# Kernel tuning notes

Hardware: AMD Instinct MI355X
Metric: run time of the kernel (lower is better)

## Reference

```python
import jax, jax.numpy as jnp
import numpy as np

B, S, H = 2, 2048, 1024
E, K, I, IS = 8, 2, 1408, 2816

def setup_inputs() -> dict:
    key = jax.random.key(0)
    ks = jax.random.split(key, 9)
    sc = lambda fan_in: 1.0 / np.sqrt(fan_in)
    return {
        'hidden_states': jax.random.normal(ks[0], (B, S, H), jnp.float32),
        'gate_w': jax.random.normal(ks[1], (H, E), jnp.float32) * sc(H),
        'w_gate': jax.random.normal(ks[2], (E, H, I), jnp.float32) * sc(H),
        'w_up': jax.random.normal(ks[3], (E, H, I), jnp.float32) * sc(H),
        'w_down': jax.random.normal(ks[4], (E, I, H), jnp.float32) * sc(I),
        'sh_gate_w': jax.random.normal(ks[5], (H, IS), jnp.float32) * sc(H),
        'sh_up_w': jax.random.normal(ks[6], (H, IS), jnp.float32) * sc(H),
        'sh_down_w': jax.random.normal(ks[7], (IS, H), jnp.float32) * sc(IS),
        'sh_expert_gate_w': jax.random.normal(ks[8], (H, 1), jnp.float32) * sc(H),
        'top_k': K,
    }

def reference(hidden_states, gate_w, w_gate, w_up, w_down, sh_gate_w, sh_up_w, sh_down_w, sh_expert_gate_w, top_k):
    orig_shape = hidden_states.shape
    x = hidden_states.reshape(-1, orig_shape[-1])  # [T, H]
    T = x.shape[0]
    n_experts = gate_w.shape[1]
    # --- routing (matches _route_single_token, no expert_bias) ---
    logits = x @ gate_w                               # [T, E]
    topk_vals, topk_ids = jax.lax.top_k(logits, top_k)  # [T, K]
    topk_weights = jax.nn.softmax(topk_vals, axis=-1)   # [T, K]
    # dense routing matrix [T, E]; each token has K nonzeros
    route = jnp.zeros((T, n_experts), x.dtype).at[jnp.arange(T)[:, None], topk_ids].add(topk_weights)
    # --- expert SwiGLU FFNs, masked-combine over the fixed expert set ---
    out = jnp.zeros_like(x)
    for e in range(n_experts):
        h = jax.nn.silu(x @ w_gate[e]) * (x @ w_up[e])  # [T, I]
        out = out + route[:, e:e + 1] * (h @ w_down[e])
    # --- shared expert (always active) with sigmoid gate ---
    shared = (jax.nn.silu(x @ sh_gate_w) * (x @ sh_up_w)) @ sh_down_w
    shared = jax.nn.sigmoid(x @ sh_expert_gate_w) * shared
    out = out + shared
    return out.reshape(orig_shape)
```

## Files before the change

### kernel.cpp

```cpp
#include <hip/hip_runtime.h>
#include <hip/hip_bf16.h>

#define T_TOK 4096
#define HDIM  1024
#define NEXP  8
#define IDIM  1408
#define ISDIM 2816
#define PADT  10240

typedef short bf16x8 __attribute__((ext_vector_type(8)));
typedef float f32x4  __attribute__((ext_vector_type(4)));
typedef unsigned short u16;
typedef unsigned short u16x4 __attribute__((ext_vector_type(4)));
typedef unsigned short u16x8 __attribute__((ext_vector_type(8)));

typedef __attribute__((address_space(1))) const void gvoid;
typedef __attribute__((address_space(3))) void lvoid;

__device__ __forceinline__ u16 f2bf(float f) {
    union { float f; unsigned u; } c; c.f = f;
    unsigned r = (c.u + 0x7FFFu + ((c.u >> 16) & 1u)) >> 16;
    return (u16)r;
}
__device__ __forceinline__ float bf2f(u16 v) {
    union { unsigned u; float f; } c; c.u = (unsigned)v << 16; return c.f;
}
__device__ __forceinline__ void glds16(const u16* g, u16* l) {
    __builtin_amdgcn_global_load_lds((gvoid*)g, (lvoid*)l, 16, 0, 0);
}

__global__ __launch_bounds__(256) void route_kernel(
    const float* __restrict__ X, const float* __restrict__ GW,
    const float* __restrict__ SEG,
    int* __restrict__ topk_e, float* __restrict__ topk_w,
    float* __restrict__ sgate)
{
    const int t = blockIdx.x * 4 + (threadIdx.x >> 6);
    const int lane = threadIdx.x & 63;
    float acc[NEXP];
    #pragma unroll
    for (int e = 0; e < NEXP; ++e) acc[e] = 0.f;
    float sacc = 0.f;
    const float* xr = X + (size_t)t * HDIM;
    for (int h = lane; h < HDIM; h += 64) {
        float xv = xr[h];
        f32x4 g0 = *(const f32x4*)(GW + (size_t)h * NEXP);
        f32x4 g1 = *(const f32x4*)(GW + (size_t)h * NEXP + 4);
        acc[0] += xv * g0[0]; acc[1] += xv * g0[1];
        acc[2] += xv * g0[2]; acc[3] += xv * g0[3];
        acc[4] += xv * g1[0]; acc[5] += xv * g1[1];
        acc[6] += xv * g1[2]; acc[7] += xv * g1[3];
        sacc += xv * SEG[h];
    }
    #pragma unroll
    for (int off = 32; off > 0; off >>= 1) {
        #pragma unroll
        for (int e = 0; e < NEXP; ++e) acc[e] += __shfl_down(acc[e], off);
        sacc += __shfl_down(sacc, off);
    }
    if (lane == 0) {
        int e0 = 0;
        #pragma unroll
        for (int e = 1; e < NEXP; ++e) if (acc[e] > acc[e0]) e0 = e;
        int e1 = (e0 == 0) ? 1 : 0;
        #pragma unroll
        for (int e = 0; e < NEXP; ++e)
            if (e != e0 && acc[e] > acc[e1]) e1 = e;
        float w0 = 1.f / (1.f + __expf(acc[e1] - acc[e0]));
        topk_e[t * 2]     = e0; topk_e[t * 2 + 1] = e1;
        topk_w[t * 2]     = w0; topk_w[t * 2 + 1] = 1.f - w0;
        sgate[t] = 1.f / (1.f + __expf(-sacc));
    }
}

__global__ __launch_bounds__(256) void hist_kernel(
    const int* __restrict__ topk_e, int* __restrict__ counts)
{
    __shared__ int h[NEXP];
    if (threadIdx.x < NEXP) h[threadIdx.x] = 0;
    __syncthreads();
    int i = blockIdx.x * 256 + threadIdx.x;
    atomicAdd(&h[topk_e[i]], 1);
    __syncthreads();
    if (threadIdx.x < NEXP) atomicAdd(&counts[threadIdx.x], h[threadIdx.x]);
}

__global__ void offsets_kernel(const int* __restrict__ counts,
                               int* __restrict__ seg_pad,
                               int* __restrict__ cursors)
{
    if (threadIdx.x == 0) {
        int s = 0;
        for (int e = 0; e < NEXP; ++e) {
            seg_pad[e] = s; cursors[e] = s;
            s += ((counts[e] + 255) >> 8) << 8;
        }
        seg_pad[NEXP] = s;
    }
}

__global__ __launch_bounds__(256) void prefill_kernel(int* __restrict__ tok_ids)
{
    int i = blockIdx.x * 256 + threadIdx.x;
    if (i < PADT) tok_ids[i] = 0;
}

__global__ __launch_bounds__(256) void scatter_kernel(
    const int* __restrict__ topk_e,
    int* __restrict__ cursors, int* __restrict__ tok_ids,
    int* __restrict__ slot)
{
    const int i = blockIdx.x * 256 + threadIdx.x;
    const int lane = threadIdx.x & 63;
    const int e = topk_e[i];
    const unsigned long long lt = (1ull << lane) - 1ull;
    #pragma unroll
    for (int ex = 0; ex < NEXP; ++ex) {
        unsigned long long mask = __ballot(e == ex);
        if (mask == 0ull) continue;
        int cnt = __popcll(mask);
        int leader = __ffsll((long long)mask) - 1;
        int base_ = 0;
        if (lane == leader) base_ = atomicAdd(&cursors[ex], cnt);
        base_ = __shfl(base_, leader);
        if (e == ex) {
            int pos = base_ + __popcll(mask & lt);
            tok_ids[pos] = i >> 1;
            slot[i] = pos;
        }
    }
}

__global__ __launch_bounds__(256) void cvt_x_kernel(
    const float* __restrict__ in, u16* __restrict__ out, int n)
{
    int i = (blockIdx.x * 256 + threadIdx.x) * 8;
    if (i < n) {
        f32x4 a = *(const f32x4*)(in + i);
        f32x4 b = *(const f32x4*)(in + i + 4);
        u16x8 o;
        #pragma unroll
        for (int j = 0; j < 4; ++j) { o[j] = f2bf(a[j]); o[j + 4] = f2bf(b[j]); }
        *(u16x8*)(out + i) = o;
    }
}

__global__ __launch_bounds__(256) void transpose_cvt(
    const float* __restrict__ in0, const float* __restrict__ in1,
    u16* __restrict__ out, int K, int N, int split, int ilv)
{
    const int z = blockIdx.z;
    const int e = (z < split) ? z : z - split;
    const float* in = (z < split) ? (in0 + (size_t)z * K * N)
                                  : (in1 + (size_t)(z - split) * K * N);
    u16* o = ilv ? (out + (size_t)e * 2 * N * K)
                 : (out + (size_t)z * N * K);
    const int radd = ilv ? ((z < split) ? 0 : 16) : 0;

    __shared__ float tile[64][65];
    const int n0 = blockIdx.x * 64, k0 = blockIdx.y * 64;
    const int tx = threadIdx.x & 15;
    const int ty = threadIdx.x >> 4;

    #pragma unroll
    for (int p = 0; p < 4; ++p) {
        int k = ty + p * 16;
        f32x4 v = *(const f32x4*)(in + (size_t)(k0 + k) * N + n0 + tx * 4);
        *(f32x4*)&tile[k][tx * 4] = v;
    }
    __syncthreads();
    #pragma unroll
    for (int p = 0; p < 4; ++p) {
        int n = ty + p * 16;
        u16x4 w;
        #pragma unroll
        for (int j = 0; j < 4; ++j) w[j] = f2bf(tile[tx * 4 + j][n]);
        int R = n0 + n;
        int orow = ilv ? (((R >> 4) * 32) + (R & 15) + radd) : R;
        *(u16x4*)(o + (size_t)orow * K + k0 + tx * 4) = w;
    }
}


#define BAR() __builtin_amdgcn_s_barrier()
#define WCNT0() asm volatile("s_waitcnt vmcnt(0)" ::: "memory")

#define GSTAGE(wb) do { \
    glds16(aP, &As[(wb) + tid * 8]); \
    glds16(bP, &Bs[(wb) + tid * 8]); \
    aP += 32; bP += 32; } while (0)

#define GEMM_TILE(rb) { \
    bf16x8 av[4], bv[4]; \
    _Pragma("unroll") for (int q = 0; q < 4; ++q) bv[q] = *(const bf16x8*)&Bs[(rb) + bofs[q]]; \
    _Pragma("unroll") for (int q = 0; q < 4; ++q) av[q] = *(const bf16x8*)&As[(rb) + aofs[q]]; \
    __builtin_amdgcn_s_setprio(1); \
    _Pragma("unroll") for (int q = 0; q < 4; ++q) \
        _Pragma("unroll") for (int w = 0; w < 4; ++w) \
            acc[q][w] = __builtin_amdgcn_mfma_f32_16x16x32_bf16(av[q], bv[w], acc[q][w], 0, 0, 0); \
    __builtin_amdgcn_s_setprio(0); }

#define GEMM_MAIN(NT) \
    GSTAGE(0); \
    _Pragma("unroll 1") \
    for (int t = 0; t < (NT) - 1; ++t) { \
        WCNT0(); BAR(); \
        GSTAGE((t & 1) ? 0 : 8192); \
        GEMM_TILE((t & 1) * 8192) \
    } \
    WCNT0(); BAR(); \
    GEMM_TILE((((NT) - 1) & 1) * 8192)

__global__ __launch_bounds__(1024, 4) void gemm_gu(
    const u16* __restrict__ A,
    const u16* __restrict__ WGUc, const u16* __restrict__ SGUc,
    u16* __restrict__ HoutE, u16* __restrict__ HoutS,
    const int* __restrict__ tok_ids, const int* __restrict__ seg_pad)
{
    extern __shared__ u16 lds[];
    u16* As = lds;
    u16* Bs = lds + 16384;

    const int zz = blockIdx.x;
    int m0, nblk, N;
    const u16* Bsrc;
    u16* Hout;
    bool gather;
    if (zz < 440) {
        int widx = zz / 11;
        nblk = zz - widx * 11;
        m0 = widx * 256;
        if (m0 >= seg_pad[NEXP]) return;
        int e = 0;
        while (e < 7 && m0 >= seg_pad[e + 1]) ++e;
        Bsrc = WGUc + (size_t)e * (2 * IDIM * HDIM);
        Hout = HoutE; N = IDIM; gather = true;
    } else {
        int sidx = zz - 440;
        int mz = sidx / 22;
        nblk = sidx - mz * 22;
        m0 = mz * 256;
        Bsrc = SGUc; Hout = HoutS; N = ISDIM; gather = false;
    }

    const int tid = threadIdx.x;
    const int srow = tid >> 2;
    const int sk = (((tid & 3) ^ ((tid >> 3) & 3))) * 8;
    const int arow = m0 + srow;
    const int ga = gather ? tok_ids[arow] : arow;
    const u16* aP = A + (size_t)ga * HDIM + sk;
    const u16* bP = Bsrc + (size_t)(nblk * 256 + srow) * HDIM + sk;

    f32x4 acc[4][4];
    #pragma unroll
    for (int i = 0; i < 4; ++i)
        #pragma unroll
        for (int j = 0; j < 4; ++j) acc[i][j] = (f32x4){0.f, 0.f, 0.f, 0.f};

    const int lane = tid & 63;
    const int wv = tid >> 6;
    const int wr = wv >> 2;
    const int wn = wv & 3;
    const int l15 = lane & 15;
    const int ksl = lane >> 4;
    const int kswz = ((ksl ^ ((l15 >> 1) & 3))) * 8;
    int aofs[4], bofs[4];
    #pragma unroll
    for (int q = 0; q < 4; ++q) {
        aofs[q] = (wr * 64 + q * 16 + l15) * 32 + kswz;
        bofs[q] = (wn * 64 + q * 16 + l15) * 32 + kswz;
    }

    GEMM_MAIN(32)

    const int l4 = ksl * 4;
    #pragma unroll
    for (int j = 0; j < 4; ++j)
        #pragma unroll
        for (int p = 0; p < 2; ++p) {
            f32x4 g = acc[j][2 * p], u = acc[j][2 * p + 1];
            int c = nblk * 128 + (wn * 2 + p) * 16 + l15;
            #pragma unroll
            for (int jj = 0; jj < 4; ++jj) {
                int r = m0 + wr * 64 + j * 16 + l4 + jj;
                float hv = g[jj] / (1.f + __expf(-g[jj])) * u[jj];
                Hout[(size_t)r * N + c] = f2bf(hv);
            }
        }
}

__global__ __launch_bounds__(1024, 4) void gemm_down(
    const u16* __restrict__ AE, const u16* __restrict__ AS,
    const u16* __restrict__ WDt, const u16* __restrict__ SDt,
    float* __restrict__ DexpO, float* __restrict__ OutS,
    const int* __restrict__ seg_pad)
{
    extern __shared__ u16 lds[];
    u16* As = lds;
    u16* Bs = lds + 16384;

    const int zz = blockIdx.x;
    const bool shr = (zz >= 160);
    int m0, n0, kst;
    size_t koff;
    const u16 *Asrc, *Bsrc;
    if (!shr) {
        int widx = zz >> 2;
        n0 = (zz & 3) * 256;
        m0 = widx * 256;
        if (m0 >= seg_pad[NEXP]) return;
        int e = 0;
        while (e < 7 && m0 >= seg_pad[e + 1]) ++e;
        Asrc = AE; Bsrc = WDt + (size_t)e * (HDIM * IDIM);
        kst = IDIM; koff = 0;
    } else {
        int idx = zz - 160;
        int kc = idx >> 6;
        int rem = idx & 63;
        m0 = (rem >> 2) * 256;
        n0 = (rem & 3) * 256;
        Asrc = AS; Bsrc = SDt;
        kst = ISDIM; koff = (size_t)kc * 1408;
    }

    const int tid = threadIdx.x;
    const int srow = tid >> 2;
    const int sk = (((tid & 3) ^ ((tid >> 3) & 3))) * 8;
    const u16* aP = Asrc + (size_t)(m0 + srow) * kst + koff + sk;
    const u16* bP = Bsrc + (size_t)(n0 + srow) * kst + koff + sk;

    f32x4 acc[4][4];
    #pragma unroll
    for (int i = 0; i < 4; ++i)
        #pragma unroll
        for (int j = 0; j < 4; ++j) acc[i][j] = (f32x4){0.f, 0.f, 0.f, 0.f};

    const int lane = tid & 63;
    const int wv = tid >> 6;
    const int wr = wv >> 2;
    const int wn = wv & 3;
    const int l15 = lane & 15;
    const int ksl = lane >> 4;
    const int kswz = ((ksl ^ ((l15 >> 1) & 3))) * 8;
    int aofs[4], bofs[4];
    #pragma unroll
    for (int q = 0; q < 4; ++q) {
        aofs[q] = (wr * 64 + q * 16 + l15) * 32 + kswz;
        bofs[q] = (wn * 64 + q * 16 + l15) * 32 + kswz;
    }

    GEMM_MAIN(44)

    const int l4 = ksl * 4;
    #pragma unroll
    for (int j = 0; j < 4; ++j)
        #pragma unroll
        for (int i = 0; i < 4; ++i) {
            int c = n0 + wn * 64 + i * 16 + l15;
            #pragma unroll
            for (int jj = 0; jj < 4; ++jj) {
                int r = m0 + wr * 64 + j * 16 + l4 + jj;
                if (!shr)
                    DexpO[(size_t)r * HDIM + c] = acc[j][i][jj];
                else
                    atomicAdd(&OutS[(size_t)r * HDIM + c], acc[j][i][jj]);
            }
        }
}

__global__ __launch_bounds__(256) void combine_kernel(
    const float* __restrict__ Dexp,
    const int* __restrict__ slot, const float* __restrict__ topk_w,
    const float* __restrict__ sgate, float* __restrict__ Out)
{
    int idx = blockIdx.x * 256 + threadIdx.x;
    int t = idx >> 8;
    int c = (idx & 255) * 4;
    int s0 = slot[2 * t], s1 = slot[2 * t + 1];
    float w0 = topk_w[2 * t], w1 = topk_w[2 * t + 1], sg = sgate[t];
    f32x4 sh = *(const f32x4*)(Out + (size_t)t * HDIM + c);
    f32x4 d0 = *(const f32x4*)(Dexp + (size_t)s0 * HDIM + c);
    f32x4 d1 = *(const f32x4*)(Dexp + (size_t)s1 * HDIM + c);
    f32x4 o;
    #pragma unroll
    for (int j = 0; j < 4; ++j) o[j] = sg * sh[j] + w0 * d0[j] + w1 * d1[j];
    *(f32x4*)(Out + (size_t)t * HDIM + c) = o;
}

extern "C" void kernel_launch(void* const* d_in, const int* in_sizes, int n_in,
                              void* d_out, int out_size, void* d_ws, size_t ws_size,
                              hipStream_t stream)
{
    const float* X   = (const float*)d_in[0];
    const float* GW  = (const float*)d_in[1];
    const float* WG  = (const float*)d_in[2];
    const float* WU  = (const float*)d_in[3];
    const float* WD  = (const float*)d_in[4];
    const float* SG  = (const float*)d_in[5];
    const float* SU  = (const float*)d_in[6];
    const float* SD  = (const float*)d_in[7];
    const float* SEG = (const float*)d_in[8];
    float* Out = (float*)d_out;

    char* ws = (char*)d_ws;
    int*   counts    = (int*)(ws + 0);
    int*   seg_pad   = (int*)(ws + 64);
    int*   cursors   = (int*)(ws + 128);
    int*   topk_e    = (int*)(ws + 1024);
    float* topk_w    = (float*)(ws + 1024 + 32768);
    float* sgate     = (float*)(ws + 1024 + 65536);
    int*   slot      = (int*)(ws + 1024 + 65536 + 16384);
    int*   tok_ids   = (int*)(ws + 1024 + 65536 + 16384 + 32768);

    u16* Xbf  = (u16*)(ws + 0x0040000ull);
    u16* Hact = (u16*)(ws + 0x0840000ull);
    u16* Hs   = (u16*)(ws + 0x23C0000ull);
    u16* WGUc = (u16*)(ws + 0x39C0000ull);
    u16* WDt  = (u16*)(ws + 0x65C0000ull);
    u16* SGUc = (u16*)(ws + 0x7BC0000ull);
    u16* SDt  = (u16*)(ws + 0x86C0000ull);
    float* Dexp = (float*)(ws + 0x39C0000ull);

    hipMemsetAsync(counts, 0, 64, stream);
    hipMemsetAsync(Out, 0, (size_t)T_TOK * HDIM * sizeof(float), stream);

    route_kernel<<<T_TOK / 4, 256, 0, stream>>>(X, GW, SEG, topk_e, topk_w, sgate);
    hist_kernel<<<(T_TOK * 2) / 256, 256, 0, stream>>>(topk_e, counts);
    offsets_kernel<<<1, 64, 0, stream>>>(counts, seg_pad, cursors);
    prefill_kernel<<<PADT / 256, 256, 0, stream>>>(tok_ids);
    scatter_kernel<<<(T_TOK * 2) / 256, 256, 0, stream>>>(topk_e, cursors, tok_ids, slot);

    cvt_x_kernel<<<(T_TOK * HDIM) / (256 * 8), 256, 0, stream>>>(X, Xbf, T_TOK * HDIM);
    transpose_cvt<<<dim3(IDIM / 64, HDIM / 64, 2 * NEXP), 256, 0, stream>>>(WG, WU, WGUc, HDIM, IDIM, NEXP, 1);
    transpose_cvt<<<dim3(HDIM / 64, IDIM / 64, NEXP), 256, 0, stream>>>(WD, WD, WDt, IDIM, HDIM, NEXP, 0);
    transpose_cvt<<<dim3(ISDIM / 64, HDIM / 64, 2), 256, 0, stream>>>(SG, SU, SGUc, HDIM, ISDIM, 1, 1);
    transpose_cvt<<<dim3(HDIM / 64, ISDIM / 64, 1), 256, 0, stream>>>(SD, SD, SDt, ISDIM, HDIM, 1, 0);

    gemm_gu<<<792, 1024, 65536, stream>>>(
        Xbf, WGUc, SGUc, Hact, Hs, tok_ids, seg_pad);

    gemm_down<<<288, 1024, 65536, stream>>>(
        Hact, Hs, WDt, SDt, Dexp, Out, seg_pad);

    combine_kernel<<<(T_TOK * HDIM / 4) / 256, 256, 0, stream>>>(
        Dexp, slot, topk_w, sgate, Out);
}
```

Before: 309.2 us.

## Remap MoE GEMM grids per expert and widen transpose-convert stores

The grouped gate/up and down GEMMs now launch a 2D grid with blockIdx.x as the expert index and blockIdx.y enumerating that expert's M and N tiles. Each block reads its expert directly from seg_pad instead of scanning segments. Shared-expert tiles are interleaved across the x dimension, which changes dispatch order and may spread work and weight reuse differently across CUs. Separately, the transpose-convert kernel writes 8 bf16 values per store instead of 4 to widen global writes. The new grid also launches more blocks that return early, and tiles past a fixed per-expert bound are dropped, which could lose work if routing is very imbalanced.

Result: slower. 321.3 us (+3.9%).

```diff
diff --git a/kernel.cpp b/kernel.cpp
--- a/kernel.cpp
+++ b/kernel.cpp
@@ -169,15 +169,17 @@
         *(f32x4*)&tile[k][tx * 4] = v;
     }
     __syncthreads();
-    #pragma unroll
-    for (int p = 0; p < 4; ++p) {
-        int n = ty + p * 16;
-        u16x4 w;
-        #pragma unroll
-        for (int j = 0; j < 4; ++j) w[j] = f2bf(tile[tx * 4 + j][n]);
+    const int kb = (threadIdx.x & 7) * 8;
+    const int nr = threadIdx.x >> 3;
+    #pragma unroll
+    for (int p = 0; p < 2; ++p) {
+        int n = nr + p * 32;
+        u16x8 w;
+        #pragma unroll
+        for (int j = 0; j < 8; ++j) w[j] = f2bf(tile[kb + j][n]);
         int R = n0 + n;
         int orow = ilv ? (((R >> 4) * 32) + (R & 15) + radd) : R;
-        *(u16x4*)(o + (size_t)orow * K + k0 + tx * 4) = w;
+        *(u16x8*)(o + (size_t)orow * K + k0 + kb) = w;
     }
 }
 
@@ -221,25 +223,27 @@
     u16* As = lds;
     u16* Bs = lds + 16384;
 
-    const int zz = blockIdx.x;
+    const int x = blockIdx.x;
+    const int y = blockIdx.y;
     int m0, nblk, N;
     const u16* Bsrc;
     u16* Hout;
     bool gather;
-    if (zz < 440) {
-        int widx = zz / 11;
-        nblk = zz - widx * 11;
-        m0 = widx * 256;
-        if (m0 >= seg_pad[NEXP]) return;
-        int e = 0;
-        while (e < 7 && m0 >= seg_pad[e + 1]) ++e;
-        Bsrc = WGUc + (size_t)e * (2 * IDIM * HDIM);
+    if (y < 176) {
+        int mt = (seg_pad[x + 1] - seg_pad[x]) >> 8;
+        if (mt == 0) return;
+        int n = y / mt;
+        if (n >= 11) return;
+        int m = y - n * mt;
+        nblk = n;
+        m0 = seg_pad[x] + m * 256;
+        Bsrc = WGUc + (size_t)x * (2 * IDIM * HDIM);
         Hout = HoutE; N = IDIM; gather = true;
     } else {
-        int sidx = zz - 440;
-        int mz = sidx / 22;
-        nblk = sidx - mz * 22;
-        m0 = mz * 256;
+        int yl = y - 176;
+        nblk = yl >> 1;
+        int ml = yl & 1;
+        m0 = (2 * x + ml) * 256;
         Bsrc = SGUc; Hout = HoutS; N = ISDIM; gather = false;
     }
 
@@ -299,26 +303,31 @@
     u16* As = lds;
     u16* Bs = lds + 16384;
 
-    const int zz = blockIdx.x;
-    const bool shr = (zz >= 160);
+    const int x = blockIdx.x;
+    const int y = blockIdx.y;
+    bool shr;
     int m0, n0, kst;
     size_t koff;
     const u16 *Asrc, *Bsrc;
-    if (!shr) {
-        int widx = zz >> 2;
-        n0 = (zz & 3) * 256;
-        m0 = widx * 256;
-        if (m0 >= seg_pad[NEXP]) return;
-        int e = 0;
-        while (e < 7 && m0 >= seg_pad[e + 1]) ++e;
-        Asrc = AE; Bsrc = WDt + (size_t)e * (HDIM * IDIM);
+    if (y < 64) {
+        shr = false;
+        int mt = (seg_pad[x + 1] - seg_pad[x]) >> 8;
+        if (mt == 0) return;
+        int n = y / mt;
+        if (n >= 4) return;
+        int m = y - n * mt;
+        m0 = seg_pad[x] + m * 256;
+        n0 = n * 256;
+        Asrc = AE; Bsrc = WDt + (size_t)x * (HDIM * IDIM);
         kst = IDIM; koff = 0;
     } else {
-        int idx = zz - 160;
-        int kc = idx >> 6;
-        int rem = idx & 63;
-        m0 = (rem >> 2) * 256;
-        n0 = (rem & 3) * 256;
+        shr = true;
+        int yl = y - 64;
+        int kc = yl >> 3;
+        int rem = yl & 7;
+        n0 = (rem >> 1) * 256;
+        int ml = rem & 1;
+        m0 = (2 * x + ml) * 256;
         Asrc = AS; Bsrc = SDt;
         kst = ISDIM; koff = (size_t)kc * 1408;
     }
@@ -436,10 +445,10 @@
     transpose_cvt<<<dim3(ISDIM / 64, HDIM / 64, 2), 256, 0, stream>>>(SG, SU, SGUc, HDIM, ISDIM, 1, 1);
     transpose_cvt<<<dim3(HDIM / 64, ISDIM / 64, 1), 256, 0, stream>>>(SD, SD, SDt, ISDIM, HDIM, 1, 0);
 
-    gemm_gu<<<792, 1024, 65536, stream>>>(
+    gemm_gu<<<dim3(8, 220), 1024, 65536, stream>>>(
         Xbf, WGUc, SGUc, Hact, Hs, tok_ids, seg_pad);
 
-    gemm_down<<<288, 1024, 65536, stream>>>(
+    gemm_down<<<dim3(8, 80), 1024, 65536, stream>>>(
         Hact, Hs, WDt, SDt, Dexp, Out, seg_pad);
 
     combine_kernel<<<(T_TOK * HDIM / 4) / 256, 256, 0, stream>>>(
```

## Fuse MoE combine into down-projection epilogue via weighted atomic scatter

Applied to the files above, without the earlier changes.

Removes the combine kernel and the Dexp intermediate buffer. The down GEMM now scales each expert row by its routing weight and atomically adds it into the output at the owning token, while the shared expert rows are scaled by the sigmoid gate. The prefill kernel is folded into the histogram kernel, which also zeroes the new per-slot weight array. The transpose-convert kernel now writes 8-wide bf16 vectors instead of 4-wide. This saves one launch and a full fp32 intermediate round trip, at the cost of more atomics, which also makes the summation order nondeterministic.

Result: slower. 372.3 us (+20.4%).

```diff
diff --git a/kernel.cpp b/kernel.cpp
--- a/kernel.cpp
+++ b/kernel.cpp
@@ -74,13 +74,15 @@
 }
 
 __global__ __launch_bounds__(256) void hist_kernel(
-    const int* __restrict__ topk_e, int* __restrict__ counts)
+    const int* __restrict__ topk_e, int* __restrict__ counts,
+    int* __restrict__ tok_ids, float* __restrict__ sw)
 {
     __shared__ int h[NEXP];
     if (threadIdx.x < NEXP) h[threadIdx.x] = 0;
     __syncthreads();
     int i = blockIdx.x * 256 + threadIdx.x;
     atomicAdd(&h[topk_e[i]], 1);
+    for (int j = i; j < PADT; j += gridDim.x * 256) { tok_ids[j] = 0; sw[j] = 0.f; }
     __syncthreads();
     if (threadIdx.x < NEXP) atomicAdd(&counts[threadIdx.x], h[threadIdx.x]);
 }
@@ -99,16 +101,10 @@
     }
 }
 
-__global__ __launch_bounds__(256) void prefill_kernel(int* __restrict__ tok_ids)
-{
-    int i = blockIdx.x * 256 + threadIdx.x;
-    if (i < PADT) tok_ids[i] = 0;
-}
-
 __global__ __launch_bounds__(256) void scatter_kernel(
-    const int* __restrict__ topk_e,
+    const int* __restrict__ topk_e, const float* __restrict__ topk_w,
     int* __restrict__ cursors, int* __restrict__ tok_ids,
-    int* __restrict__ slot)
+    float* __restrict__ sw)
 {
     const int i = blockIdx.x * 256 + threadIdx.x;
     const int lane = threadIdx.x & 63;
@@ -126,7 +122,7 @@
         if (e == ex) {
             int pos = base_ + __popcll(mask & lt);
             tok_ids[pos] = i >> 1;
-            slot[i] = pos;
+            sw[pos] = topk_w[i];
         }
     }
 }
@@ -169,15 +165,17 @@
         *(f32x4*)&tile[k][tx * 4] = v;
     }
     __syncthreads();
-    #pragma unroll
-    for (int p = 0; p < 4; ++p) {
-        int n = ty + p * 16;
-        u16x4 w;
-        #pragma unroll
-        for (int j = 0; j < 4; ++j) w[j] = f2bf(tile[tx * 4 + j][n]);
+    const int kb = (threadIdx.x & 7) * 8;
+    const int nr = threadIdx.x >> 3;
+    #pragma unroll
+    for (int p = 0; p < 2; ++p) {
+        int n = nr + p * 32;
+        u16x8 w;
+        #pragma unroll
+        for (int j = 0; j < 8; ++j) w[j] = f2bf(tile[kb + j][n]);
         int R = n0 + n;
         int orow = ilv ? (((R >> 4) * 32) + (R & 15) + radd) : R;
-        *(u16x4*)(o + (size_t)orow * K + k0 + tx * 4) = w;
+        *(u16x8*)(o + (size_t)orow * K + k0 + kb) = w;
     }
 }
 
@@ -292,7 +290,9 @@
 __global__ __launch_bounds__(1024, 4) void gemm_down(
     const u16* __restrict__ AE, const u16* __restrict__ AS,
     const u16* __restrict__ WDt, const u16* __restrict__ SDt,
-    float* __restrict__ DexpO, float* __restrict__ OutS,
+    float* __restrict__ Out,
+    const int* __restrict__ tok_ids, const float* __restrict__ sw,
+    const float* __restrict__ sgate,
     const int* __restrict__ seg_pad)
 {
     extern __shared__ u16 lds[];
@@ -360,31 +360,15 @@
             #pragma unroll
             for (int jj = 0; jj < 4; ++jj) {
                 int r = m0 + wr * 64 + j * 16 + l4 + jj;
-                if (!shr)
-                    DexpO[(size_t)r * HDIM + c] = acc[j][i][jj];
-                else
-                    atomicAdd(&OutS[(size_t)r * HDIM + c], acc[j][i][jj]);
+                if (!shr) {
+                    float w = sw[r];
+                    int tok = tok_ids[r];
+                    atomicAdd(&Out[(size_t)tok * HDIM + c], w * acc[j][i][jj]);
+                } else {
+                    atomicAdd(&Out[(size_t)r * HDIM + c], sgate[r] * acc[j][i][jj]);
+                }
             }
         }
-}
-
-__global__ __launch_bounds__(256) void combine_kernel(
-    const float* __restrict__ Dexp,
-    const int* __restrict__ slot, const float* __restrict__ topk_w,
-    const float* __restrict__ sgate, float* __restrict__ Out)
-{
-    int idx = blockIdx.x * 256 + threadIdx.x;
-    int t = idx >> 8;
-    int c = (idx & 255) * 4;
-    int s0 = slot[2 * t], s1 = slot[2 * t + 1];
-    float w0 = topk_w[2 * t], w1 = topk_w[2 * t + 1], sg = sgate[t];
-    f32x4 sh = *(const f32x4*)(Out + (size_t)t * HDIM + c);
-    f32x4 d0 = *(const f32x4*)(Dexp + (size_t)s0 * HDIM + c);
-    f32x4 d1 = *(const f32x4*)(Dexp + (size_t)s1 * HDIM + c);
-    f32x4 o;
-    #pragma unroll
-    for (int j = 0; j < 4; ++j) o[j] = sg * sh[j] + w0 * d0[j] + w1 * d1[j];
-    *(f32x4*)(Out + (size_t)t * HDIM + c) = o;
 }
 
 extern "C" void kernel_launch(void* const* d_in, const int* in_sizes, int n_in,
@@ -409,8 +393,8 @@
     int*   topk_e    = (int*)(ws + 1024);
     float* topk_w    = (float*)(ws + 1024 + 32768);
     float* sgate     = (float*)(ws + 1024 + 65536);
-    int*   slot      = (int*)(ws + 1024 + 65536 + 16384);
-    int*   tok_ids   = (int*)(ws + 1024 + 65536 + 16384 + 32768);
+    int*   tok_ids   = (int*)(ws + 1024 + 65536 + 16384);
+    float* sw        = (float*)(ws + 1024 + 65536 + 16384 + 40960);
 
     u16* Xbf  = (u16*)(ws + 0x0040000ull);
     u16* Hact = (u16*)(ws + 0x0840000ull);
@@ -419,16 +403,14 @@
     u16* WDt  = (u16*)(ws + 0x65C0000ull);
     u16* SGUc = (u16*)(ws + 0x7BC0000ull);
     u16* SDt  = (u16*)(ws + 0x86C0000ull);
-    float* Dexp = (float*)(ws + 0x39C0000ull);
 
     hipMemsetAsync(counts, 0, 64, stream);
     hipMemsetAsync(Out, 0, (size_t)T_TOK * HDIM * sizeof(float), stream);
 
     route_kernel<<<T_TOK / 4, 256, 0, stream>>>(X, GW, SEG, topk_e, topk_w, sgate);
-    hist_kernel<<<(T_TOK * 2) / 256, 256, 0, stream>>>(topk_e, counts);
+    hist_kernel<<<(T_TOK * 2) / 256, 256, 0, stream>>>(topk_e, counts, tok_ids, sw);
     offsets_kernel<<<1, 64, 0, stream>>>(counts, seg_pad, cursors);
-    prefill_kernel<<<PADT / 256, 256, 0, stream>>>(tok_ids);
-    scatter_kernel<<<(T_TOK * 2) / 256, 256, 0, stream>>>(topk_e, cursors, tok_ids, slot);
+    scatter_kernel<<<(T_TOK * 2) / 256, 256, 0, stream>>>(topk_e, topk_w, cursors, tok_ids, sw);
 
     cvt_x_kernel<<<(T_TOK * HDIM) / (256 * 8), 256, 0, stream>>>(X, Xbf, T_TOK * HDIM);
     transpose_cvt<<<dim3(IDIM / 64, HDIM / 64, 2 * NEXP), 256, 0, stream>>>(WG, WU, WGUc, HDIM, IDIM, NEXP, 1);
@@ -440,8 +422,5 @@
         Xbf, WGUc, SGUc, Hact, Hs, tok_ids, seg_pad);
 
     gemm_down<<<288, 1024, 65536, stream>>>(
-        Hact, Hs, WDt, SDt, Dexp, Out, seg_pad);
-
-    combine_kernel<<<(T_TOK * HDIM / 4) / 256, 256, 0, stream>>>(
-        Dexp, slot, topk_w, sgate, Out);
-}
+        Hact, Hs, WDt, SDt, Out, tok_ids, sw, sgate, seg_pad);
+}
```
